# Optimization experiments

Measured on AMD Instinct MI355X. Metric: run time of the kernel, lower is better.

The kernel has to match this reference:

```python
import jax, jax.numpy as jnp
import numpy as np

N, E, D, A, M, H, NRES = 65536, 16384, 1024, 512, 2048, 3, 3


def setup_inputs() -> dict:
    key = jax.random.key(0)
    ks = jax.random.split(key, 24)
    s = 0.02
    inp = {
        'h': jax.random.normal(ks[0], (N, D), dtype=jnp.float32),
        'rep': jax.random.normal(ks[1], (N, D), dtype=jnp.float32),
        'src': jax.random.randint(ks[2], (E,), 0, N, dtype=jnp.int32),
        'dst': jax.random.randint(ks[3], (E,), 0, N, dtype=jnp.int32),
        # per-head attention projections (stacked over H heads)
        'Wq': s * jax.random.normal(ks[4], (H, D, A), dtype=jnp.float32),
        'bq': s * jax.random.normal(ks[5], (H, A), dtype=jnp.float32),
        'Wk': s * jax.random.normal(ks[6], (H, D, A), dtype=jnp.float32),
        'bk': s * jax.random.normal(ks[7], (H, A), dtype=jnp.float32),
        'Wv': s * jax.random.normal(ks[8], (H, D, A), dtype=jnp.float32),
        'bv': s * jax.random.normal(ks[9], (H, A), dtype=jnp.float32),
        # MultiMLPLayer: first Linear(A->M), then NRES ResNet blocks of width M
        'W0': s * jax.random.normal(ks[10], (H, A, M), dtype=jnp.float32),
        'b0': s * jax.random.normal(ks[11], (H, M), dtype=jnp.float32),
        'Wr': s * jax.random.normal(ks[12], (H, NRES, M, M), dtype=jnp.float32),
        'br': s * jax.random.normal(ks[13], (H, NRES, M), dtype=jnp.float32),
        'g_ln': jnp.ones((H, NRES, M), dtype=jnp.float32),
        'b_ln': jnp.zeros((H, NRES, M), dtype=jnp.float32),
        # mlp_scale: Linear(M->A) per head
        'Wms': s * jax.random.normal(ks[14], (H, M, A), dtype=jnp.float32),
        'bms': s * jax.random.normal(ks[15], (H, A), dtype=jnp.float32),
        # update_attn_scale: Linear(H*A -> D, bias=False)
        'Wuas': s * jax.random.normal(ks[16], (H * A, D), dtype=jnp.float32),
    }
    return inp


def _layernorm(x, g, b, eps=1e-5):
    mu = jnp.mean(x, axis=-1, keepdims=True)
    var = jnp.mean((x - mu) ** 2, axis=-1, keepdims=True)
    return (x - mu) / jnp.sqrt(var + eps) * g + b


def reference(h, rep, src, dst, Wq, bq, Wk, bk, Wv, bv, W0, b0, Wr, br,
              g_ln, b_ln, Wms, bms, Wuas):
    # model normalizes all node embeddings first (F.normalize)
    hn = h / jnp.maximum(jnp.linalg.norm(h, axis=-1, keepdims=True), 1e-12)
    Q = hn[src]            # [E, D] mailbox messages (copy_u of 'h')
    K = rep[dst]           # [E, D] destination node reps (K == V)

    # per-head projections: [H, E, A]
    Qp = jnp.einsum('ed,hda->hea', Q, Wq) + bq[:, None, :]
    Kp = jnp.einsum('ed,hda->hea', K, Wk) + bk[:, None, :]
    Vp = jnp.einsum('ed,hda->hea', K, Wv) + bv[:, None, :]

    attn_dim = Wq.shape[-1]
    scores = (Qp * Kp) / (attn_dim ** 0.5)       # 2D path: elementwise QK, scaled by sqrt(attn_size)
    attn = jax.nn.softmax(scores, axis=-1)       # softmax over feature dim
    attn_out = attn * Vp                         # [H, E, A] (dropout p=0.0 in TreeHopNode)

    # MultiMLPLayer: Linear(A->M) then NRES ResNet blocks
    m = jnp.einsum('hea,ham->hem', attn_out, W0) + b0[:, None, :]
    for j in range(Wr.shape[1]):
        xn = _layernorm(m, g_ln[:, j][:, None, :], b_ln[:, j][:, None, :])
        m = m + jax.nn.relu(jnp.einsum('hem,hmn->hen', xn, Wr[:, j]) + br[:, j][:, None, :])

    head_out = jnp.einsum('hem,hma->hea', m, Wms) + bms[:, None, :] + attn_out  # [H, E, A]
    cat = jnp.transpose(head_out, (1, 0, 2)).reshape(Q.shape[0], -1)            # [E, H*A]

    # reduce_func: h = Q - K + update_attn_scale(multi_head_out)
    return Q - K + cat @ Wuas                                                   # [E, D]
```

## Files before the change

kernel.cpp:

```cpp
#include <hip/hip_runtime.h>
#include <hip/hip_bf16.h>
#include <cstdint>
#include <cstddef>

typedef __bf16 bf16;
typedef __bf16 bf16x2 __attribute__((ext_vector_type(2)));
typedef __bf16 bf16x4 __attribute__((ext_vector_type(4)));
typedef __bf16 bf16x8 __attribute__((ext_vector_type(8)));
typedef float f32x4 __attribute__((ext_vector_type(4)));

static_assert(sizeof(bf16x8) == 16, "bf16x8 must be 16B");

#define NE 16384
#define ND 1024
#define NA 512
#define NM 2048
#define NH 3
#define NRES 3

__device__ __forceinline__ void async_ld16(const bf16* g, bf16* l) {
  __builtin_amdgcn_global_load_lds(
      (__attribute__((address_space(1))) void*)(void*)g,
      (__attribute__((address_space(3))) void*)(void*)l, 16, 0, 0);
}

template <int N>
__device__ __forceinline__ void vm_wait() {
  asm volatile("s_waitcnt vmcnt(%0)" ::"n"(N) : "memory");
}
__device__ __forceinline__ void lgkm0() {
  asm volatile("s_waitcnt lgkmcnt(0)" ::: "memory");
}
__device__ __forceinline__ void bar() {
  asm volatile("s_barrier" ::: "memory");
}
#define PIN() __builtin_amdgcn_sched_barrier(0)


#define LDA_H(KS, BUF, MQ)                                                    \
  {                                                                           \
    const int ab_ = ((BUF)*2 + (MQ)) * 8192 + aOff;                           \
    const int co_ = (c0 ^ ((KS) << 2)) * 8;                                   \
    _Pragma("unroll") for (int i = 0; i < 4; ++i)                             \
        fa[KS][i] = *(const bf16x8*)&lA[ab_ + i * 1024 + co_];                \
  }

#define LDB_H(DST, KS, BUF, NQ)                                               \
  {                                                                           \
    const int bb_ = ((BUF)*2 + (NQ)) * 8192 + bOff;                           \
    const int co_ = (c0 ^ ((KS) << 2)) * 8;                                   \
    _Pragma("unroll") for (int j = 0; j < 2; ++j)                             \
        DST[KS][j] = *(const bf16x8*)&lB[bb_ + j * 1024 + co_];               \
  }

#define MFMA_H(KS, MQ, NQ, FB)                                                \
  __builtin_amdgcn_s_setprio(1);                                              \
  _Pragma("unroll") for (int i = 0; i < 4; ++i)                               \
  _Pragma("unroll") for (int j = 0; j < 2; ++j)                               \
      acc[(MQ)*4 + i][(NQ)*2 + j] = __builtin_amdgcn_mfma_f32_16x16x32_bf16(  \
          fa[KS][i], FB[KS][j], acc[(MQ)*4 + i][(NQ)*2 + j], 0, 0, 0);        \
  __builtin_amdgcn_s_setprio(0);

template <int MODE>
__global__ __launch_bounds__(512, 2) void gemm_kernel(
    const bf16* __restrict__ A, const bf16* __restrict__ B,
    const float* __restrict__ bias, void* __restrict__ Cv,
    const bf16* __restrict__ addb, int K, int ldc, int coloff, int addld,
    int nbx) {
  __shared__ bf16 lA[32768];
  __shared__ bf16 lB[32768];

  const int nwg = gridDim.x;
  int bid = blockIdx.x;
  if ((nwg & 7) == 0) bid = (bid & 7) * (nwg >> 3) + (bid >> 3);
  const int n0 = (bid % nbx) * 256;
  const int m0 = (bid / nbx) * 256;

  const int tid = threadIdx.x;
  const int wv = tid >> 6, ln = tid & 63;
  const int wm = wv >> 2, wn = wv & 3;

  const int rowq = wv * 8 + (ln >> 3);
  const int colo = ((ln & 7) ^ (ln >> 3)) * 8;
  const bf16* gA = A + (size_t)(m0 + rowq) * K + colo;
  const bf16* gB = B + (size_t)(n0 + rowq) * K + colo;

  auto stageA = [&](int bf, int u, int t) {
#pragma unroll
    for (int r = 0; r < 2; ++r)
      async_ld16(gA + (size_t)(r * 128 + u * 64) * K + t * 64,
                 &lA[((bf * 2 + u) * 128 + r * 64 + wv * 8) * 64]);
  };
  auto stageB = [&](int bf, int u, int t) {
#pragma unroll
    for (int r = 0; r < 2; ++r)
      async_ld16(gB + (size_t)(r * 128 + u * 64) * K + t * 64,
                 &lB[((bf * 2 + u) * 128 + r * 64 + wv * 8) * 64]);
  };

  const int l15 = ln & 15;
  const int aOff = (wm * 64 + l15) * 64;
  const int bOff = (wn * 32 + l15) * 64;
  const int c0 = (ln >> 4) ^ (ln & 7);

  f32x4 acc[8][4] = {};
  bf16x8 fa[2][4], fb0[2][2], fb1[2][2];

  const int nt = K >> 6;

  stageA(0, 0, 0); stageA(0, 1, 0); stageB(0, 0, 0); stageB(0, 1, 0);
  stageA(1, 0, 1); stageA(1, 1, 1); stageB(1, 0, 1); stageB(1, 1, 1);
  vm_wait<8>();
  bar();
  LDA_H(0, 0, 0); LDA_H(1, 0, 0); LDB_H(fb0, 0, 0, 0); LDB_H(fb0, 1, 0, 0);
  lgkm0();
  bar();

  for (int t = 0; t < nt; ++t) {
    const int buf = t & 1, nb = buf ^ 1;
    const bool s1 = t + 1 < nt, s2 = t + 2 < nt;
    if (s2) { stageB(buf, 0, t + 2); stageA(buf, 0, t + 2); }
    PIN();
    LDB_H(fb1, 0, buf, 1); LDB_H(fb1, 1, buf, 1);
    PIN();
    MFMA_H(0, 0, 0, fb0);
    MFMA_H(1, 0, 0, fb0);
    MFMA_H(0, 0, 1, fb1);
    PIN();
    LDA_H(0, buf, 1);
    PIN();
    MFMA_H(1, 0, 1, fb1);
    PIN();
    LDA_H(1, buf, 1);
    lgkm0();
    bar();
    if (s2) { stageB(buf, 1, t + 2); stageA(buf, 1, t + 2); }
    PIN();
    MFMA_H(0, 1, 1, fb1);
    MFMA_H(1, 1, 1, fb1);
    if (s2) { vm_wait<8>(); } else if (s1) { vm_wait<0>(); }
    bar();
    MFMA_H(0, 1, 0, fb0);
    PIN();
    if (s1) { LDB_H(fb0, 0, nb, 0); LDA_H(0, nb, 0); }
    PIN();
    MFMA_H(1, 1, 0, fb0);
    PIN();
    if (s1) { LDB_H(fb0, 1, nb, 0); LDA_H(1, nb, 0); }
    lgkm0();
    bar();
  }

  const int r4 = (ln >> 4) * 4;
  const int nbase = n0 + (wn >> 1) * 128 + (wn & 1) * 32 + l15;
#pragma unroll
  for (int mi = 0; mi < 8; ++mi) {
#pragma unroll
    for (int ni = 0; ni < 4; ++ni) {
#pragma unroll
      for (int r = 0; r < 4; ++r) {
        const int m = m0 + wm * 128 + mi * 16 + r4 + r;
        const int n = nbase + (ni >> 1) * 64 + (ni & 1) * 16;
        float v = acc[mi][ni][r];
        if constexpr (MODE != 3) v += bias[n];
        if constexpr (MODE == 0) {
          size_t idx = (size_t)m * ldc + n;
          if (coloff && n >= coloff) idx += (size_t)addld;
          ((bf16*)Cv)[idx] = (bf16)v;
        } else if constexpr (MODE == 1) {
          float prev = (float)addb[(size_t)m * addld + n];
          ((bf16*)Cv)[(size_t)m * ldc + n] = (bf16)(prev + fmaxf(v, 0.f));
        } else if constexpr (MODE == 2) {
          v += (float)addb[(size_t)m * addld + n];
          ((bf16*)Cv)[(size_t)m * ldc + coloff + n] = (bf16)v;
        } else {
          float* C = (float*)Cv;
          const size_t idx = (size_t)m * ldc + n;
          C[idx] = C[idx] + v;
        }
      }
    }
  }
}

template <int MODE>
static void launch_gemm(hipStream_t s, const bf16* A, const bf16* B,
                        const float* bias, void* C, const bf16* addb, int M,
                        int N, int K, int ldc, int coloff, int addld) {
  const int nbx = N / 256;
  gemm_kernel<MODE><<<dim3(nbx * (M / 256)), 512, 0, s>>>(
      A, B, bias, C, addb, K, ldc, coloff, addld, nbx);
}

__global__ void transpose_cvt(const float* __restrict__ src,
                              bf16* __restrict__ dst, int K, int N) {
  __shared__ float t[32][33];
  const size_t zo = (size_t)blockIdx.z * K * N;
  src += zo;
  dst += zo;
  const int n = blockIdx.x * 32 + threadIdx.x;
  const int kb = blockIdx.y * 32;
#pragma unroll
  for (int i = 0; i < 4; ++i) {
    const int k = kb + threadIdx.y + i * 8;
    t[threadIdx.y + i * 8][threadIdx.x] = src[(size_t)k * N + n];
  }
  __syncthreads();
#pragma unroll
  for (int i = 0; i < 4; ++i) {
    const int nn = blockIdx.x * 32 + threadIdx.y + i * 8;
    dst[(size_t)nn * K + kb + threadIdx.x] =
        (bf16)t[threadIdx.x][threadIdx.y + i * 8];
  }
}

__global__ void concat2_kernel(const float* __restrict__ a,
                               const float* __restrict__ b,
                               float* __restrict__ dst, int na) {
  const int i = blockIdx.x * 256 + threadIdx.x;
  dst[i] = (i < na) ? a[i] : b[i - na];
}

__global__ __launch_bounds__(256) void gather_kernel(
    const float* __restrict__ h, const float* __restrict__ rep,
    const int* __restrict__ src, const int* __restrict__ dst,
    bf16* __restrict__ Qb, bf16* __restrict__ Kb, float* __restrict__ qk) {
  __shared__ float sm[4];
  const int e = blockIdx.x, tid = threadIdx.x;
  const int sr = src[e], dr = dst[e];
  const float4 hv = ((const float4*)(h + (size_t)sr * ND))[tid];
  float ss = hv.x * hv.x + hv.y * hv.y + hv.z * hv.z + hv.w * hv.w;
#pragma unroll
  for (int o = 32; o > 0; o >>= 1) ss += __shfl_down(ss, o, 64);
  if ((tid & 63) == 0) sm[tid >> 6] = ss;
  __syncthreads();
  const float tot = sm[0] + sm[1] + sm[2] + sm[3];
  const float inv = 1.f / fmaxf(sqrtf(tot), 1e-12f);
  const float4 rv = ((const float4*)(rep + (size_t)dr * ND))[tid];
  const float q0 = hv.x * inv, q1 = hv.y * inv, q2 = hv.z * inv,
              q3 = hv.w * inv;
  const size_t base = (size_t)e * ND + tid * 4;
  bf16x4 qv;
  qv[0] = (bf16)q0; qv[1] = (bf16)q1; qv[2] = (bf16)q2; qv[3] = (bf16)q3;
  *(bf16x4*)(Qb + base) = qv;
  bf16x4 kv;
  kv[0] = (bf16)rv.x; kv[1] = (bf16)rv.y; kv[2] = (bf16)rv.z;
  kv[3] = (bf16)rv.w;
  *(bf16x4*)(Kb + base) = kv;
  *(float4*)(qk + base) =
      make_float4(q0 - rv.x, q1 - rv.y, q2 - rv.z, q3 - rv.w);
}

__global__ __launch_bounds__(256) void softmax_kernel(
    const bf16* __restrict__ Qp, const bf16* __restrict__ Kp,
    const bf16* __restrict__ Vp, bf16* __restrict__ attn) {
  __shared__ float sm[4];
  const int tid = threadIdx.x;
  const int e = blockIdx.x, hh = blockIdx.y;
  const size_t base = (size_t)e * (NH * NA) + (size_t)hh * NA + 2 * tid;
  const bf16x2 q = *(const bf16x2*)(Qp + base);
  const bf16x2 k = *(const bf16x2*)(Kp + base);
  const bf16x2 v = *(const bf16x2*)(Vp + base);
  const float sc = 0.044194173824159216f;
  const float s0 = (float)q[0] * (float)k[0] * sc;
  const float s1 = (float)q[1] * (float)k[1] * sc;
  float mx = fmaxf(s0, s1);
#pragma unroll
  for (int o = 32; o > 0; o >>= 1) mx = fmaxf(mx, __shfl_down(mx, o, 64));
  if ((tid & 63) == 0) sm[tid >> 6] = mx;
  __syncthreads();
  mx = fmaxf(fmaxf(sm[0], sm[1]), fmaxf(sm[2], sm[3]));
  __syncthreads();
  const float p0 = expf(s0 - mx), p1 = expf(s1 - mx);
  float ssum = p0 + p1;
#pragma unroll
  for (int o = 32; o > 0; o >>= 1) ssum += __shfl_down(ssum, o, 64);
  if ((tid & 63) == 0) sm[tid >> 6] = ssum;
  __syncthreads();
  const float inv = 1.f / (sm[0] + sm[1] + sm[2] + sm[3]);
  bf16x2 r;
  r[0] = (bf16)(p0 * inv * (float)v[0]);
  r[1] = (bf16)(p1 * inv * (float)v[1]);
  const size_t obase = (size_t)hh * NE * NA + (size_t)e * NA + 2 * tid;
  *(bf16x2*)(attn + obase) = r;
}

__global__ __launch_bounds__(256) void ln_kernel(const bf16* __restrict__ x,
                                                 bf16* __restrict__ y,
                                                 const float* __restrict__ g,
                                                 const float* __restrict__ b) {
  __shared__ float sm[8];
  const int tid = threadIdx.x;
  const size_t base = (size_t)blockIdx.x * NM + tid * 8;
  const bf16x8 xv = *(const bf16x8*)(x + base);
  float xf[8], s = 0.f, ss = 0.f;
#pragma unroll
  for (int i = 0; i < 8; ++i) {
    xf[i] = (float)xv[i];
    s += xf[i];
    ss += xf[i] * xf[i];
  }
#pragma unroll
  for (int o = 32; o > 0; o >>= 1) {
    s += __shfl_down(s, o, 64);
    ss += __shfl_down(ss, o, 64);
  }
  if ((tid & 63) == 0) {
    sm[tid >> 6] = s;
    sm[4 + (tid >> 6)] = ss;
  }
  __syncthreads();
  s = sm[0] + sm[1] + sm[2] + sm[3];
  ss = sm[4] + sm[5] + sm[6] + sm[7];
  const float mu = s * (1.f / NM);
  const float var = ss * (1.f / NM) - mu * mu;
  const float rstd = rsqrtf(fmaxf(var, 0.f) + 1e-5f);
  const int c0 = tid * 8;
  bf16x8 yv;
#pragma unroll
  for (int i = 0; i < 8; ++i)
    yv[i] = (bf16)((xf[i] - mu) * rstd * g[c0 + i] + b[c0 + i]);
  *(bf16x8*)(y + base) = yv;
}

extern "C" void kernel_launch(void* const* d_in, const int* in_sizes, int n_in,
                              void* d_out, int out_size, void* d_ws,
                              size_t ws_size, hipStream_t stream) {
  const float* h    = (const float*)d_in[0];
  const float* rep  = (const float*)d_in[1];
  const int* src    = (const int*)d_in[2];
  const int* dst    = (const int*)d_in[3];
  const float* Wq   = (const float*)d_in[4];
  const float* bq   = (const float*)d_in[5];
  const float* Wk   = (const float*)d_in[6];
  const float* bk   = (const float*)d_in[7];
  const float* Wv   = (const float*)d_in[8];
  const float* bv   = (const float*)d_in[9];
  const float* W0   = (const float*)d_in[10];
  const float* b0   = (const float*)d_in[11];
  const float* Wr   = (const float*)d_in[12];
  const float* br   = (const float*)d_in[13];
  const float* g_ln = (const float*)d_in[14];
  const float* b_ln = (const float*)d_in[15];
  const float* Wms  = (const float*)d_in[16];
  const float* bms  = (const float*)d_in[17];
  const float* Wuas = (const float*)d_in[18];
  float* out = (float*)d_out;

  bf16* ws = (bf16*)d_ws;
  size_t off = 0;
  auto alloc = [&](size_t n) {
    bf16* p = ws + off;
    off += n;
    return p;
  };
  bf16* WqT   = alloc((size_t)NH * NA * ND);
  bf16* WkT   = alloc((size_t)NH * NA * ND);
  bf16* WvT   = alloc((size_t)NH * NA * ND);
  bf16* W0T   = alloc((size_t)NH * NM * NA);
  bf16* WrT   = alloc((size_t)NH * NRES * NM * NM);
  bf16* WmsT  = alloc((size_t)NH * NA * NM);
  bf16* WuasT = alloc((size_t)ND * NH * NA);
  bf16* Qb    = alloc((size_t)NE * ND);
  bf16* Kb    = alloc((size_t)NE * ND);
  bf16* Qp    = alloc((size_t)NE * NH * NA);
  bf16* Kp    = alloc((size_t)NE * NH * NA);
  bf16* Vp    = alloc((size_t)NE * NH * NA);
  bf16* attn  = alloc((size_t)NH * NE * NA);
  bf16* mbuf  = alloc((size_t)NE * NM);
  bf16* xnb   = alloc((size_t)NE * NM);
  float* cbias = (float*)alloc(2 * (size_t)NH * NA * 2);
  bf16* cat   = Qp;
  if (ws_size < off * sizeof(bf16)) return;

  const dim3 tb(32, 8);
  transpose_cvt<<<dim3(NA / 32, ND / 32, NH), tb, 0, stream>>>(Wq, WqT, ND, NA);
  transpose_cvt<<<dim3(NA / 32, ND / 32, NH), tb, 0, stream>>>(Wk, WkT, ND, NA);
  transpose_cvt<<<dim3(NA / 32, ND / 32, NH), tb, 0, stream>>>(Wv, WvT, ND, NA);
  transpose_cvt<<<dim3(NM / 32, NA / 32, NH), tb, 0, stream>>>(W0, W0T, NA, NM);
  transpose_cvt<<<dim3(NM / 32, NM / 32, NH * NRES), tb, 0, stream>>>(Wr, WrT,
                                                                      NM, NM);
  transpose_cvt<<<dim3(NA / 32, NM / 32, NH), tb, 0, stream>>>(Wms, WmsT, NM,
                                                               NA);
  transpose_cvt<<<dim3(ND / 32, (NH * NA) / 32, 1), tb, 0, stream>>>(
      Wuas, WuasT, NH * NA, ND);
  concat2_kernel<<<(2 * NH * NA) / 256, 256, 0, stream>>>(bk, bv, cbias,
                                                          NH * NA);

  gather_kernel<<<NE, 256, 0, stream>>>(h, rep, src, dst, Qb, Kb, out);

  launch_gemm<0>(stream, Qb, WqT, bq, Qp, nullptr, NE, NH * NA, ND, NH * NA,
                 0, 0);
  launch_gemm<0>(stream, Kb, WkT, cbias, Kp, nullptr, NE, 2 * NH * NA, ND,
                 NH * NA, NH * NA, (NE - 1) * NH * NA);
  softmax_kernel<<<dim3(NE, NH), 256, 0, stream>>>(Qp, Kp, Vp, attn);

  for (int hh = 0; hh < NH; ++hh) {
    const bf16* attn_h = attn + (size_t)hh * NE * NA;
    launch_gemm<0>(stream, attn_h, W0T + (size_t)hh * NM * NA, b0 + hh * NM,
                   mbuf, nullptr, NE, NM, NA, NM, 0, 0);
    for (int j = 0; j < NRES; ++j) {
      const int hj = hh * NRES + j;
      ln_kernel<<<NE, 256, 0, stream>>>(mbuf, xnb, g_ln + (size_t)hj * NM,
                                        b_ln + (size_t)hj * NM);
      launch_gemm<1>(stream, xnb, WrT + (size_t)hj * NM * NM, br + hj * NM,
                     mbuf, mbuf, NE, NM, NM, NM, 0, NM);
    }
    launch_gemm<2>(stream, mbuf, WmsT + (size_t)hh * NA * NM, bms + hh * NA,
                   cat, attn_h, NE, NA, NM, NH * NA, hh * NA, NA);
  }
  launch_gemm<3>(stream, cat, WuasT, nullptr, out, nullptr, NE, ND, NH * NA,
                 ND, 0, 0);
}
```

Before: 2.692 ms.

## Restructure GEMM main loop into barrier-separated load/MFMA phases

Rewrites the K-loop schedule of the bf16 MFMA GEMM. Cross-iteration register prefetch of the next buffer's fragments and the sched_barrier pins are dropped. Each iteration now loads its own LDS fragments in four phases, each followed by barriers and a prioritized MFMA cluster, with global-to-LDS staging interleaved between phases. The aim is a ping-pong style overlap between waves that simplifies scheduling. In exchange it adds more barriers and no longer hides LDS read latency across iterations.

```diff
diff --git a/kernel.cpp b/kernel.cpp
--- a/kernel.cpp
+++ b/kernel.cpp
@@ -34,7 +34,6 @@
 __device__ __forceinline__ void bar() {
   asm volatile("s_barrier" ::: "memory");
 }
-#define PIN() __builtin_amdgcn_sched_barrier(0)
 
 
 #define LDA_H(KS, BUF, MQ)                                                    \
@@ -54,11 +53,15 @@
   }
 
 #define MFMA_H(KS, MQ, NQ, FB)                                                \
-  __builtin_amdgcn_s_setprio(1);                                              \
   _Pragma("unroll") for (int i = 0; i < 4; ++i)                               \
   _Pragma("unroll") for (int j = 0; j < 2; ++j)                               \
       acc[(MQ)*4 + i][(NQ)*2 + j] = __builtin_amdgcn_mfma_f32_16x16x32_bf16(  \
-          fa[KS][i], FB[KS][j], acc[(MQ)*4 + i][(NQ)*2 + j], 0, 0, 0);        \
+          fa[KS][i], FB[KS][j], acc[(MQ)*4 + i][(NQ)*2 + j], 0, 0, 0);
+
+#define MFMA_PH(MQ, NQ, FB)                                                   \
+  __builtin_amdgcn_s_setprio(1);                                              \
+  MFMA_H(0, MQ, NQ, FB);                                                      \
+  MFMA_H(1, MQ, NQ, FB);                                                      \
   __builtin_amdgcn_s_setprio(0);
 
 template <int MODE>
@@ -108,46 +111,37 @@
 
   const int nt = K >> 6;
 
-  stageA(0, 0, 0); stageA(0, 1, 0); stageB(0, 0, 0); stageB(0, 1, 0);
-  stageA(1, 0, 1); stageA(1, 1, 1); stageB(1, 0, 1); stageB(1, 1, 1);
+  stageB(0, 0, 0); stageA(0, 0, 0); stageB(0, 1, 0); stageA(0, 1, 0);
+  stageB(1, 0, 1); stageA(1, 0, 1); stageB(1, 1, 1); stageA(1, 1, 1);
   vm_wait<8>();
   bar();
-  LDA_H(0, 0, 0); LDA_H(1, 0, 0); LDB_H(fb0, 0, 0, 0); LDB_H(fb0, 1, 0, 0);
-  lgkm0();
-  bar();
 
   for (int t = 0; t < nt; ++t) {
-    const int buf = t & 1, nb = buf ^ 1;
-    const bool s1 = t + 1 < nt, s2 = t + 2 < nt;
+    const int buf = t & 1;
+    const bool s2 = t + 2 < nt;
+    LDA_H(0, buf, 0); LDA_H(1, buf, 0);
+    LDB_H(fb0, 0, buf, 0); LDB_H(fb0, 1, buf, 0);
+    bar();
+    lgkm0();
+    MFMA_PH(0, 0, fb0);
+    bar();
+    LDB_H(fb1, 0, buf, 1); LDB_H(fb1, 1, buf, 1);
     if (s2) { stageB(buf, 0, t + 2); stageA(buf, 0, t + 2); }
-    PIN();
-    LDB_H(fb1, 0, buf, 1); LDB_H(fb1, 1, buf, 1);
-    PIN();
-    MFMA_H(0, 0, 0, fb0);
-    MFMA_H(1, 0, 0, fb0);
-    MFMA_H(0, 0, 1, fb1);
-    PIN();
-    LDA_H(0, buf, 1);
-    PIN();
-    MFMA_H(1, 0, 1, fb1);
-    PIN();
-    LDA_H(1, buf, 1);
+    bar();
     lgkm0();
-    bar();
-    if (s2) { stageB(buf, 1, t + 2); stageA(buf, 1, t + 2); }
-    PIN();
-    MFMA_H(0, 1, 1, fb1);
-    MFMA_H(1, 1, 1, fb1);
-    if (s2) { vm_wait<8>(); } else if (s1) { vm_wait<0>(); }
-    bar();
-    MFMA_H(0, 1, 0, fb0);
-    PIN();
-    if (s1) { LDB_H(fb0, 0, nb, 0); LDA_H(0, nb, 0); }
-    PIN();
-    MFMA_H(1, 1, 0, fb0);
-    PIN();
-    if (s1) { LDB_H(fb0, 1, nb, 0); LDA_H(1, nb, 0); }
+    MFMA_PH(0, 1, fb1);
+    bar();
+    LDA_H(0, buf, 1); LDA_H(1, buf, 1);
+    if (s2) stageB(buf, 1, t + 2);
+    bar();
     lgkm0();
+    MFMA_PH(1, 1, fb1);
+    bar();
+    if (s2) { stageA(buf, 1, t + 2); vm_wait<8>(); }
+    else { vm_wait<0>(); }
+    bar();
+    lgkm0();
+    MFMA_PH(1, 0, fb0);
     bar();
   }
 
```

New measurement: 2.716 ms. About the same (+0.9%).

## Batch per-head MLP GEMMs and layernorms into single launches across heads

Applied to the files above, without the earlier changes.

Replaces the per-head loop of MLP GEMMs and layernorm kernels with single launches covering all three heads stacked along M. Each workgroup derives its head index from its row offset and offsets the weight and bias pointers, and the output column offset, to match. The aim is to cut launch count and give each GEMM three times as many workgroups, which should fill the GPU better and reduce tail effects. In exchange the intermediate buffers grow to hold all heads at once, using more workspace memory.

```diff
diff --git a/kernel.cpp b/kernel.cpp
--- a/kernel.cpp
+++ b/kernel.cpp
@@ -17,6 +17,7 @@
 #define NM 2048
 #define NH 3
 #define NRES 3
+#define ESH 14
 
 __device__ __forceinline__ void async_ld16(const bf16* g, bf16* l) {
   __builtin_amdgcn_global_load_lds(
@@ -66,7 +67,7 @@
     const bf16* __restrict__ A, const bf16* __restrict__ B,
     const float* __restrict__ bias, void* __restrict__ Cv,
     const bf16* __restrict__ addb, int K, int ldc, int coloff, int addld,
-    int nbx) {
+    int nbx, int hsh, long long bstr, int bistr) {
   __shared__ bf16 lA[32768];
   __shared__ bf16 lB[32768];
 
@@ -75,6 +76,12 @@
   if ((nwg & 7) == 0) bid = (bid & 7) * (nwg >> 3) + (bid >> 3);
   const int n0 = (bid % nbx) * 256;
   const int m0 = (bid / nbx) * 256;
+
+  const int hidx = hsh ? (m0 >> hsh) : 0;
+  if (hsh) {
+    B += (size_t)hidx * (size_t)bstr;
+    bias += (size_t)hidx * (size_t)bistr;
+  }
 
   const int tid = threadIdx.x;
   const int wv = tid >> 6, ln = tid & 63;
@@ -172,7 +179,8 @@
           ((bf16*)Cv)[(size_t)m * ldc + n] = (bf16)(prev + fmaxf(v, 0.f));
         } else if constexpr (MODE == 2) {
           v += (float)addb[(size_t)m * addld + n];
-          ((bf16*)Cv)[(size_t)m * ldc + coloff + n] = (bf16)v;
+          const int mloc = hsh ? (m & ((1 << hsh) - 1)) : m;
+          ((bf16*)Cv)[(size_t)mloc * ldc + hidx * coloff + n] = (bf16)v;
         } else {
           float* C = (float*)Cv;
           const size_t idx = (size_t)m * ldc + n;
@@ -186,10 +194,11 @@
 template <int MODE>
 static void launch_gemm(hipStream_t s, const bf16* A, const bf16* B,
                         const float* bias, void* C, const bf16* addb, int M,
-                        int N, int K, int ldc, int coloff, int addld) {
+                        int N, int K, int ldc, int coloff, int addld,
+                        int hsh = 0, long long bstr = 0, int bistr = 0) {
   const int nbx = N / 256;
   gemm_kernel<MODE><<<dim3(nbx * (M / 256)), 512, 0, s>>>(
-      A, B, bias, C, addb, K, ldc, coloff, addld, nbx);
+      A, B, bias, C, addb, K, ldc, coloff, addld, nbx, hsh, bstr, bistr);
 }
 
 __global__ void transpose_cvt(const float* __restrict__ src,
@@ -288,9 +297,11 @@
 __global__ __launch_bounds__(256) void ln_kernel(const bf16* __restrict__ x,
                                                  bf16* __restrict__ y,
                                                  const float* __restrict__ g,
-                                                 const float* __restrict__ b) {
+                                                 const float* __restrict__ b,
+                                                 int hstr) {
   __shared__ float sm[8];
   const int tid = threadIdx.x;
+  const int hb = (blockIdx.x >> ESH) * hstr;
   const size_t base = (size_t)blockIdx.x * NM + tid * 8;
   const bf16x8 xv = *(const bf16x8*)(x + base);
   float xf[8], s = 0.f, ss = 0.f;
@@ -319,7 +330,7 @@
   bf16x8 yv;
 #pragma unroll
   for (int i = 0; i < 8; ++i)
-    yv[i] = (bf16)((xf[i] - mu) * rstd * g[c0 + i] + b[c0 + i]);
+    yv[i] = (bf16)((xf[i] - mu) * rstd * g[hb + c0 + i] + b[hb + c0 + i]);
   *(bf16x8*)(y + base) = yv;
 }
 
@@ -367,8 +378,8 @@
   bf16* Kp    = alloc((size_t)NE * NH * NA);
   bf16* Vp    = alloc((size_t)NE * NH * NA);
   bf16* attn  = alloc((size_t)NH * NE * NA);
-  bf16* mbuf  = alloc((size_t)NE * NM);
-  bf16* xnb   = alloc((size_t)NE * NM);
+  bf16* mbuf3 = alloc((size_t)NH * NE * NM);
+  bf16* xnb3  = alloc((size_t)NH * NE * NM);
   float* cbias = (float*)alloc(2 * (size_t)NH * NA * 2);
   bf16* cat   = Qp;
   if (ws_size < off * sizeof(bf16)) return;
@@ -395,20 +406,19 @@
                  NH * NA, NH * NA, (NE - 1) * NH * NA);
   softmax_kernel<<<dim3(NE, NH), 256, 0, stream>>>(Qp, Kp, Vp, attn);
 
-  for (int hh = 0; hh < NH; ++hh) {
-    const bf16* attn_h = attn + (size_t)hh * NE * NA;
-    launch_gemm<0>(stream, attn_h, W0T + (size_t)hh * NM * NA, b0 + hh * NM,
-                   mbuf, nullptr, NE, NM, NA, NM, 0, 0);
-    for (int j = 0; j < NRES; ++j) {
-      const int hj = hh * NRES + j;
-      ln_kernel<<<NE, 256, 0, stream>>>(mbuf, xnb, g_ln + (size_t)hj * NM,
-                                        b_ln + (size_t)hj * NM);
-      launch_gemm<1>(stream, xnb, WrT + (size_t)hj * NM * NM, br + hj * NM,
-                     mbuf, mbuf, NE, NM, NM, NM, 0, NM);
-    }
-    launch_gemm<2>(stream, mbuf, WmsT + (size_t)hh * NA * NM, bms + hh * NA,
-                   cat, attn_h, NE, NA, NM, NH * NA, hh * NA, NA);
-  }
+  launch_gemm<0>(stream, attn, W0T, b0, mbuf3, nullptr, NH * NE, NM, NA, NM,
+                 0, 0, ESH, (long long)NM * NA, NM);
+  for (int j = 0; j < NRES; ++j) {
+    ln_kernel<<<NH * NE, 256, 0, stream>>>(mbuf3, xnb3,
+                                           g_ln + (size_t)j * NM,
+                                           b_ln + (size_t)j * NM, NRES * NM);
+    launch_gemm<1>(stream, xnb3, WrT + (size_t)j * NM * NM,
+                   br + (size_t)j * NM, mbuf3, mbuf3, NH * NE, NM, NM, NM, 0,
+                   NM, ESH, (long long)NRES * NM * NM, NRES * NM);
+  }
+  launch_gemm<2>(stream, mbuf3, WmsT, bms, cat, attn, NH * NE, NA, NM,
+                 NH * NA, NA, NA, ESH, (long long)NA * NM, NA);
+
   launch_gemm<3>(stream, cat, WuasT, nullptr, out, nullptr, NE, ND, NH * NA,
                  ND, 0, 0);
 }
```

Measured after the change: 2.838 ms. 1.05x slower.
